# Kernel tuning notes

Measured on AMD Instinct MI355X. Metric: run time of the kernel, lower is better.

## Reference

```python
import jax, jax.numpy as jnp
import numpy as np

B, L, D, DFF, MODES = 16, 1536, 512, 2048, 64
KERNELS = (3, 5, 7)


def setup_inputs() -> dict:
    key = jax.random.key(0)
    ks = jax.random.split(key, 12)
    scale = 1.0 / (D * D)
    f32 = jnp.float32
    return {
        "x": jax.random.normal(ks[0], (B, L, D), f32),
        "w_real": scale * jax.random.normal(ks[1], (D, D, MODES), f32),
        "w_imag": scale * jax.random.normal(ks[2], (D, D, MODES), f32),
        "conv1_w": jax.random.normal(ks[3], (DFF, D), f32) / np.sqrt(D).astype(np.float32),
        "conv2_w": jax.random.normal(ks[4], (D, DFF), f32) / np.sqrt(DFF).astype(np.float32),
        "d1_w1": jax.random.normal(ks[5], (D // 2, D), f32) / np.sqrt(D).astype(np.float32),
        "d1_b1": jnp.zeros((D // 2,), f32),
        "d1_w2": jax.random.normal(ks[6], (len(KERNELS), D // 2), f32) / np.sqrt(D // 2).astype(np.float32),
        "d1_b2": jnp.zeros((len(KERNELS),), f32),
        "d2_w1": jax.random.normal(ks[7], (D // 2, D), f32) / np.sqrt(D).astype(np.float32),
        "d2_b1": jnp.zeros((D // 2,), f32),
        "d2_w2": jax.random.normal(ks[8], (len(KERNELS), D // 2), f32) / np.sqrt(D // 2).astype(np.float32),
        "d2_b2": jnp.zeros((len(KERNELS),), f32),
    }


def _avg_pool1d(x, k):
    # torch AvgPool1d(kernel=k, stride=1, padding=k//2), count_include_pad=True:
    # zero-pad then divide by k everywhere. x: (B, L, D) -> (B, L, D) for odd k.
    pad = k // 2
    xp = jnp.pad(x, ((0, 0), (pad, pad), (0, 0)))
    cs = jnp.pad(jnp.cumsum(xp, axis=1), ((0, 0), (1, 0), (0, 0)))
    return (cs[:, k:, :] - cs[:, :-k, :]) / k


def _moe_decomp(x, w1, b1, w2, b2):
    # trends: (B, L, D, E)
    trends = jnp.stack([_avg_pool1d(x, k) for k in KERNELS], axis=-1)
    h = jax.nn.relu(jnp.einsum("bld,hd->blh", x, w1) + b1)
    logits = jnp.einsum("blh,eh->ble", h, w2) + b2
    gates = jax.nn.softmax(logits, axis=-1)[:, :, None, :]  # (B, L, 1, E)
    x_trend = jnp.sum(trends * gates, axis=-1)
    return x - x_trend  # seasonal component


def _fourier_block(x, w_real, w_imag):
    q_ft = jnp.fft.rfft(x, axis=1)  # (B, L//2+1, D) complex
    modes = min(MODES, q_ft.shape[1])
    weights = (w_real + 1j * w_imag).astype(jnp.complex64)  # (D, D, modes)
    # batched complex matmul over the kept modes (fuses the per-mode loop)
    out_m = jnp.einsum("bmd,dem->bme", q_ft[:, :modes, :], weights[:, :, :modes])
    out_ft = jnp.zeros((x.shape[0], x.shape[1] // 2 + 1, x.shape[2]), jnp.complex64)
    out_ft = out_ft.at[:, :modes, :].set(out_m)
    return jnp.fft.irfft(out_ft, n=x.shape[1], axis=1)


def reference(x, w_real, w_imag, conv1_w, conv2_w,
              d1_w1, d1_b1, d1_w2, d1_b2,
              d2_w1, d2_b1, d2_w2, d2_b2):
    # FEB-f + residual (dropout = identity in eval)
    x = x + _fourier_block(x, w_real, w_imag)
    x = _moe_decomp(x, d1_w1, d1_b1, d1_w2, d1_b2)
    # 1x1 conv FFN == per-token linear layers
    y = jax.nn.relu(jnp.einsum("bld,fd->blf", x, conv1_w))
    y = jnp.einsum("blf,df->bld", y, conv2_w)
    res = _moe_decomp(x + y, d2_w1, d2_b1, d2_w2, d2_b2)
    return res
```

## Files before the change

### kernel.cpp

```cpp
#include <hip/hip_runtime.h>

#define B_   16
#define L_   1536
#define D_   512
#define DFF_ 2048
#define NM   64
#define HID  256

typedef short short8  __attribute__((ext_vector_type(8)));
typedef short short4v __attribute__((ext_vector_type(4)));
typedef float f32x4   __attribute__((ext_vector_type(4)));

__device__ __forceinline__ float b2f(short s) {
  unsigned int u = ((unsigned int)(unsigned short)s) << 16;
  float f; __builtin_memcpy(&f, &u, 4); return f;
}
__device__ __forceinline__ short f2b(float f) {
  unsigned int u; __builtin_memcpy(&u, &f, 4);
  u += 0x7fffu + ((u >> 16) & 1u);
  return (short)(u >> 16);
}
__device__ __forceinline__ f32x4 zero4() {
  f32x4 v; v[0]=0.f; v[1]=0.f; v[2]=0.f; v[3]=0.f; return v;
}

#define MFMA(a,b,c) __builtin_amdgcn_mfma_f32_16x16x32_bf16((a),(b),(c),0,0,0)
#define SWZ(row, grp) (((row) << 6) + ((((grp) ^ ((row) & 7))) << 3))
#define GLDS16(gp, lp) __builtin_amdgcn_global_load_lds( \
    (const __attribute__((address_space(1))) void*)(gp), \
    (__attribute__((address_space(3))) void*)(lp), 16, 0, 0)

__global__ __launch_bounds__(256) void zero_out(float* __restrict__ o, int n) {
  int i = blockIdx.x * 256 + threadIdx.x;
  if (i < n) o[i] = 0.f;
}

__global__ __launch_bounds__(256) void cvt_f32_bf16(const float* __restrict__ s,
                                                    short* __restrict__ d, int n4) {
  int i = blockIdx.x * 256 + threadIdx.x;
  if (i >= n4) return;
  f32x4 v = ((const f32x4*)s)[i];
  short4v o;
  #pragma unroll
  for (int j = 0; j < 4; ++j) o[j] = f2b(v[j]);
  ((short4v*)d)[i] = o;
}

__global__ __launch_bounds__(256) void build_tcs(short* __restrict__ tcs) {
  int i = blockIdx.x * 256 + threadIdx.x;
  if (i >= 128 * L_) return;
  int m = i / L_, l = i - m * L_;
  int mm = (m < 64) ? m : (m - 64);
  int r = (mm * l) % L_;
  float th = (float)r * (6.283185307179586f / (float)L_);
  float s, c; __sincosf(th, &s, &c);
  tcs[i] = f2b((m < 64) ? c : -s);
}
__global__ __launch_bounds__(256) void build_basis(short* __restrict__ basis) {
  int i = blockIdx.x * 256 + threadIdx.x;
  if (i >= L_ * 128) return;
  int l = i >> 7, k = i & 127;
  int m = (k < 64) ? k : (k - 64);
  int r = (m * l) % L_;
  float th = (float)r * (6.283185307179586f / (float)L_);
  float s, c; __sincosf(th, &s, &c);
  float v = (k < 64) ? ((m == 0) ? 1.f : 2.f) * (1.f / (float)L_) * c
                     : (-2.f / (float)L_) * s;
  basis[i] = f2b(v);
}

__global__ __launch_bounds__(256) void transpose_w(const float* __restrict__ w,
                                                   short* __restrict__ wt) {
  __shared__ float tile[64][17];
  int dc = blockIdx.x, e = blockIdx.y, t = threadIdx.x;
  int mBase = blockIdx.z * 16;
  {
    int dl = t >> 2, mg = t & 3;
    f32x4 v = *(const f32x4*)(w + ((long)(dc * 64 + dl) * 512 + e) * 64 + mBase + mg * 4);
    tile[dl][mg*4+0] = v[0]; tile[dl][mg*4+1] = v[1];
    tile[dl][mg*4+2] = v[2]; tile[dl][mg*4+3] = v[3];
  }
  __syncthreads();
  if (t < 128) {
    int mr = t >> 3, dg = t & 7;
    short8 o;
    #pragma unroll
    for (int j = 0; j < 8; ++j) o[j] = f2b(tile[dg * 8 + j][mr]);
    *(short8*)(wt + ((long)(mBase + mr) * 512 + e) * 512 + dc * 64 + dg * 8) = o;
  }
}

__global__ __launch_bounds__(256) void transpose_x(const float* __restrict__ x,
                                                   short* __restrict__ xt) {
  __shared__ float tile[64][65];
  int dc = blockIdx.x, lc = blockIdx.y, b = blockIdx.z, t = threadIdx.x;
  const float* xb = x + (long)b * L_ * D_;
  #pragma unroll
  for (int i = 0; i < 4; ++i) {
    int idx = i * 256 + t; int ll = idx >> 4, dg = idx & 15;
    f32x4 v = *(const f32x4*)(xb + (long)(lc * 64 + ll) * D_ + dc * 64 + dg * 4);
    tile[ll][dg*4+0] = v[0]; tile[ll][dg*4+1] = v[1];
    tile[ll][dg*4+2] = v[2]; tile[ll][dg*4+3] = v[3];
  }
  __syncthreads();
  #pragma unroll
  for (int i = 0; i < 2; ++i) {
    int idx = i * 256 + t; int dl = idx >> 3, lg = idx & 7;
    short8 o;
    #pragma unroll
    for (int j = 0; j < 8; ++j) o[j] = f2b(tile[lg * 8 + j][dl]);
    *(short8*)(xt + ((long)b * D_ + dc * 64 + dl) * L_ + lc * 64 + lg * 8) = o;
  }
}

__global__ __launch_bounds__(256) void transpose_q(const short* __restrict__ in,
                                                   short* __restrict__ out) {
  __shared__ short tile[64][72];
  int ct = blockIdx.x, rt = blockIdx.y, t = threadIdx.x;
  int r0 = rt * 64, c0 = ct * 64;
  #pragma unroll
  for (int i = 0; i < 2; ++i) {
    int idx = i * 256 + t; int r = idx >> 3, g = idx & 7;
    short8 v = *(const short8*)(in + (long)(r0 + r) * 128 + c0 + g * 8);
    #pragma unroll
    for (int j = 0; j < 8; ++j) tile[r][g * 8 + j] = v[j];
  }
  __syncthreads();
  #pragma unroll
  for (int i = 0; i < 2; ++i) {
    int idx = i * 256 + t; int c = idx >> 3, g = idx & 7;
    short8 o;
    #pragma unroll
    for (int j = 0; j < 8; ++j) o[j] = tile[g * 8 + j][c];
    *(short8*)(out + (long)(c0 + c) * 8192 + r0 + g * 8) = o;
  }
}

template<bool RELU, bool HASBIAS>
__global__ __launch_bounds__(256) void gemm64(
    const short* __restrict__ A, long ldA,
    const short* __restrict__ W, long ldW,
    const float* __restrict__ bias,
    short* __restrict__ outB, long ldC, int K)
{
  __shared__ short lA[64 * 64];
  __shared__ short lW[64 * 64];
  const int t = threadIdx.x, lane = t & 63, wid = t >> 6;
  const int quad = lane >> 4, l15 = lane & 15;
  const int wm = (wid & 1) * 32, wn = (wid >> 1) * 32;
  const long row0 = (long)blockIdx.x * 64, col0 = (long)blockIdx.y * 64;
  const short* Ab = A + row0 * ldA;
  const short* Wb = W + col0 * ldW;

  int srcrow[2]; long srcoff[2];
  #pragma unroll
  for (int i = 0; i < 2; ++i) {
    int c = wid * 2 + i;
    int r = c * 8 + (lane >> 3);
    int g = (lane & 7) ^ (r & 7);
    srcrow[i] = r; srcoff[i] = g * 8;
  }

  f32x4 acc[2][2];
  #pragma unroll
  for (int i = 0; i < 2; ++i)
    #pragma unroll
    for (int j = 0; j < 2; ++j) acc[i][j] = zero4();

  for (int k0 = 0; k0 < K; k0 += 64) {
    __syncthreads();
    #pragma unroll
    for (int i = 0; i < 2; ++i) {
      int c = wid * 2 + i;
      GLDS16(Ab + (long)srcrow[i] * ldA + k0 + srcoff[i], lA + c * 512);
      GLDS16(Wb + (long)srcrow[i] * ldW + k0 + srcoff[i], lW + c * 512);
    }
    __syncthreads();
    #pragma unroll
    for (int ks = 0; ks < 2; ++ks) {
      int gq = ks * 4 + quad;
      short8 a0 = *(const short8*)&lA[SWZ(wm + l15, gq)];
      short8 a1 = *(const short8*)&lA[SWZ(wm + 16 + l15, gq)];
      short8 b0 = *(const short8*)&lW[SWZ(wn + l15, gq)];
      short8 b1 = *(const short8*)&lW[SWZ(wn + 16 + l15, gq)];
      acc[0][0] = MFMA(a0, b0, acc[0][0]);
      acc[0][1] = MFMA(a0, b1, acc[0][1]);
      acc[1][0] = MFMA(a1, b0, acc[1][0]);
      acc[1][1] = MFMA(a1, b1, acc[1][1]);
    }
  }
  #pragma unroll
  for (int ni = 0; ni < 2; ++ni) {
    long col = col0 + wn + ni * 16 + l15;
    float bvv = HASBIAS ? bias[col] : 0.f;
    #pragma unroll
    for (int mi = 0; mi < 2; ++mi) {
      #pragma unroll
      for (int r = 0; r < 4; ++r) {
        long row = row0 + wm + mi * 16 + quad * 4 + r;
        float v = acc[mi][ni][r];
        if (HASBIAS) v += bvv;
        if (RELU)    v = fmaxf(v, 0.f);
        outB[row * ldC + col] = f2b(v);
      }
    }
  }
}

template<bool RELU, bool HASBIAS, bool HASRES, bool RESB>
__global__ __launch_bounds__(256) void gemm128(
    const short* __restrict__ A, long ldA, long Az,
    const short* __restrict__ W, long ldW, long Wz,
    const float* __restrict__ bias,
    const void* __restrict__ res, long ldres, long resZ,
    short* __restrict__ outB, long ldC, long Cz, int K)
{
  __shared__ short lA[128 * 64];
  __shared__ short lW[128 * 64];
  const int t = threadIdx.x, lane = t & 63, wid = t >> 6;
  const int quad = lane >> 4, l15 = lane & 15;
  const int wm = (wid & 1) * 64, wn = (wid >> 1) * 64;
  const long row0 = (long)blockIdx.x * 128, col0 = (long)blockIdx.y * 128;
  const int z = blockIdx.z;
  const short* Ab = A + (long)z * Az + row0 * ldA;
  const short* Wb = W + (long)z * Wz + col0 * ldW;

  int srcrow[4]; long srcoff[4];
  #pragma unroll
  for (int i = 0; i < 4; ++i) {
    int c = wid * 4 + i;
    int r = c * 8 + (lane >> 3);
    int g = (lane & 7) ^ (r & 7);
    srcrow[i] = r; srcoff[i] = g * 8;
  }

  f32x4 acc[4][4];
  #pragma unroll
  for (int i = 0; i < 4; ++i)
    #pragma unroll
    for (int j = 0; j < 4; ++j) acc[i][j] = zero4();

  for (int k0 = 0; k0 < K; k0 += 64) {
    __syncthreads();
    #pragma unroll
    for (int i = 0; i < 4; ++i) {
      int c = wid * 4 + i;
      GLDS16(Ab + (long)srcrow[i] * ldA + k0 + srcoff[i], lA + c * 512);
      GLDS16(Wb + (long)srcrow[i] * ldW + k0 + srcoff[i], lW + c * 512);
    }
    __syncthreads();
    #pragma unroll
    for (int ks = 0; ks < 2; ++ks) {
      int gq = ks * 4 + quad;
      short8 av[4], bv[4];
      #pragma unroll
      for (int mi = 0; mi < 4; ++mi) av[mi] = *(const short8*)&lA[SWZ(wm + mi * 16 + l15, gq)];
      #pragma unroll
      for (int ni = 0; ni < 4; ++ni) bv[ni] = *(const short8*)&lW[SWZ(wn + ni * 16 + l15, gq)];
      #pragma unroll
      for (int mi = 0; mi < 4; ++mi)
        #pragma unroll
        for (int ni = 0; ni < 4; ++ni)
          acc[mi][ni] = MFMA(av[mi], bv[ni], acc[mi][ni]);
    }
  }
  #pragma unroll
  for (int ni = 0; ni < 4; ++ni) {
    long col = col0 + wn + ni * 16 + l15;
    float bvv = HASBIAS ? bias[col] : 0.f;
    #pragma unroll
    for (int mi = 0; mi < 4; ++mi) {
      #pragma unroll
      for (int r = 0; r < 4; ++r) {
        long row = row0 + wm + mi * 16 + quad * 4 + r;
        float v = acc[mi][ni][r];
        if (HASBIAS) v += bvv;
        if (RELU)    v = fmaxf(v, 0.f);
        if (HASRES) {
          long ro = (long)z * resZ + row * ldres + col;
          v += RESB ? b2f(((const short*)res)[ro]) : ((const float*)res)[ro];
        }
        outB[(long)z * Cz + row * ldC + col] = f2b(v);
      }
    }
  }
}

__global__ __launch_bounds__(256) void mode_gemm(
    const short* __restrict__ qr, const short* __restrict__ qi,
    const short* __restrict__ wr, const short* __restrict__ wi,
    short* __restrict__ outm)
{
  __shared__ short lqr[16 * 64], lqi[16 * 64], lwr[64 * 64], lwi[64 * 64];
  const int m = blockIdx.x, en = blockIdx.y;
  const int t = threadIdx.x, lane = t & 63, wid = t >> 6;
  const int quad = lane >> 4, l15 = lane & 15;
  const short* qrb = qr + (long)m * (B_ * D_);
  const short* qib = qi + (long)m * (B_ * D_);
  const short* wrb = wr + (long)m * (D_ * D_) + (long)en * 64 * D_;
  const short* wib = wi + (long)m * (D_ * D_) + (long)en * 64 * D_;
  f32x4 accr = zero4(), acci = zero4();
  for (int k0 = 0; k0 < D_; k0 += 64) {
    __syncthreads();
    {
      int idx = t & 127; int r = idx >> 3, cg = idx & 7;
      const short* src = (t < 128 ? qrb : qib) + r * D_ + k0 + cg * 8;
      short* dst = (t < 128) ? lqr : lqi;
      *(short8*)&dst[SWZ(r, cg)] = *(const short8*)src;
    }
    #pragma unroll
    for (int i = 0; i < 4; ++i) {
      int idx = i * 256 + t;
      int which = idx >> 9, idx2 = idx & 511;
      int r = idx2 >> 3, cg = idx2 & 7;
      const short* src = (which ? wib : wrb) + r * D_ + k0 + cg * 8;
      short* dst = which ? lwi : lwr;
      *(short8*)&dst[SWZ(r, cg)] = *(const short8*)src;
    }
    __syncthreads();
    #pragma unroll
    for (int ks = 0; ks < 2; ++ks) {
      int gq = ks * 4 + quad;
      short8 ar = *(const short8*)&lqr[SWZ(l15, gq)];
      short8 ai = *(const short8*)&lqi[SWZ(l15, gq)];
      short8 br = *(const short8*)&lwr[SWZ(wid * 16 + l15, gq)];
      short8 bi = *(const short8*)&lwi[SWZ(wid * 16 + l15, gq)];
      short8 nai;
      #pragma unroll
      for (int j = 0; j < 8; ++j) nai[j] = (short)(ai[j] ^ (short)0x8000);
      accr = MFMA(ar, br, accr);
      accr = MFMA(nai, bi, accr);
      acci = MFMA(ar, bi, acci);
      acci = MFMA(ai, br, acci);
    }
  }
  #pragma unroll
  for (int r = 0; r < 4; ++r) {
    int bb = quad * 4 + r;
    long e = (long)en * 64 + wid * 16 + l15;
    long base = ((long)bb * D_ + e) * 128 + m;
    outm[base]      = f2b(accr[r]);
    outm[base + 64] = f2b(acci[r]);
  }
}

__global__ __launch_bounds__(256) void gates_kernel(
    const short* __restrict__ h, const float* __restrict__ w2,
    const float* __restrict__ b2, float* __restrict__ g, int rows)
{
  int wid = threadIdx.x >> 6, lane = threadIdx.x & 63;
  int row = blockIdx.x * 4 + wid;
  if (row >= rows) return;
  const short* hr = h + (long)row * HID;
  short4v hh = *(const short4v*)(hr + lane * 4);
  float hv[4];
  #pragma unroll
  for (int j = 0; j < 4; ++j) hv[j] = b2f(hh[j]);
  float lg[3];
  #pragma unroll
  for (int e = 0; e < 3; ++e) {
    const float* wrow = w2 + e * HID + lane * 4;
    float p = hv[0] * wrow[0] + hv[1] * wrow[1] + hv[2] * wrow[2] + hv[3] * wrow[3];
    #pragma unroll
    for (int off = 32; off >= 1; off >>= 1) p += __shfl_xor(p, off);
    lg[e] = p + b2[e];
  }
  float mx = fmaxf(lg[0], fmaxf(lg[1], lg[2]));
  float e0 = __expf(lg[0] - mx), e1 = __expf(lg[1] - mx), e2 = __expf(lg[2] - mx);
  float inv = 1.f / (e0 + e1 + e2);
  float gv = (lane == 0) ? e0 * inv : (lane == 1) ? e1 * inv : e2 * inv;
  if (lane < 3) g[(long)row * 3 + lane] = gv;
}

template<bool OUTF, bool WRITEB>
__global__ __launch_bounds__(512) void combine_kernel(
    const short* __restrict__ xin, const float* __restrict__ g,
    float* __restrict__ outf, short* __restrict__ outb)
{
  int lc = blockIdx.x, b = blockIdx.y, d = threadIdx.x;
  int l0 = lc * 64;
  const short* xb = xin + (long)b * L_ * D_ + d;
  const float* gb = g + (long)b * L_ * 3;
  float win[7];
  #pragma unroll
  for (int j = 0; j < 6; ++j) {
    int l = l0 - 3 + j;
    win[j] = (l >= 0 && l < L_) ? b2f(xb[(long)l * D_]) : 0.f;
  }
  for (int i = 0; i < 64; ++i) {
    int lcn = l0 + i;
    int lr = lcn + 3;
    win[6] = (lr < L_) ? b2f(xb[(long)lr * D_]) : 0.f;
    float s3 = win[2] + win[3] + win[4];
    float s5 = s3 + win[1] + win[5];
    float s7 = s5 + win[0] + win[6];
    float g0 = gb[lcn * 3 + 0], g1 = gb[lcn * 3 + 1], g2 = gb[lcn * 3 + 2];
    float trend = g0 * s3 * (1.f / 3.f) + g1 * s5 * (1.f / 5.f) + g2 * s7 * (1.f / 7.f);
    float v = win[3] - trend;
    long o = ((long)b * L_ + lcn) * D_ + d;
    if (OUTF)   outf[o] = v;
    if (WRITEB) outb[o] = f2b(v);
    #pragma unroll
    for (int j = 0; j < 6; ++j) win[j] = win[j + 1];
  }
}

extern "C" void kernel_launch(void* const* d_in, const int* in_sizes, int n_in,
                              void* d_out, int out_size, void* d_ws, size_t ws_size,
                              hipStream_t stream) {
  const float* x       = (const float*)d_in[0];
  const float* w_real  = (const float*)d_in[1];
  const float* w_imag  = (const float*)d_in[2];
  const float* conv1_w = (const float*)d_in[3];
  const float* conv2_w = (const float*)d_in[4];
  const float* d1_w1   = (const float*)d_in[5];
  const float* d1_b1   = (const float*)d_in[6];
  const float* d1_w2   = (const float*)d_in[7];
  const float* d1_b2   = (const float*)d_in[8];
  const float* d2_w1   = (const float*)d_in[9];
  const float* d2_b1   = (const float*)d_in[10];
  const float* d2_w2   = (const float*)d_in[11];
  const float* d2_b2   = (const float*)d_in[12];
  float* OUT = (float*)d_out;

  const size_t REQ_BIG = 144703488, REQ_SMALL = 98566144;
  if (ws_size < REQ_SMALL) {
    zero_out<<<(out_size + 255) / 256, 256, 0, stream>>>(OUT, out_size);
    return;
  }
  const bool big = (ws_size >= REQ_BIG);

  char* ws = (char*)d_ws;
  short* C1WB  = (short*)(ws + 0);
  short* C2WB  = (short*)(ws + 2097152);
  short* D1W1B = (short*)(ws + 4194304);
  short* D2W1B = (short*)(ws + 4456448);
  short* TCS   = (short*)(ws + 4718592);
  short* BASIS = (short*)(ws + 5111808);
  float* G     = (float*)(ws + 5505024);
  short* XT    = (short*)(ws + 6291456);
  short* QRI   = XT;
  short* Y1    = XT;
  short* QT    = (short*)(ws + 31457280);
  short* OUTM  = (short*)(ws + 33554432);
  short* WTR   = (short*)(ws + 35651584);
  short* X1B   = WTR;
  short* WTI   = (short*)(ws + 69206016);
  short* X2B   = (short*)(ws + (big ? 106954752 : 60817408));
  short* H     = (short*)(ws + (big ? 132120576 : 85983232));

  cvt_f32_bf16<<<(262144 + 255) / 256, 256, 0, stream>>>(conv1_w, C1WB, 262144);
  cvt_f32_bf16<<<(262144 + 255) / 256, 256, 0, stream>>>(conv2_w, C2WB, 262144);
  cvt_f32_bf16<<<(32768 + 255) / 256, 256, 0, stream>>>(d1_w1, D1W1B, 32768);
  cvt_f32_bf16<<<(32768 + 255) / 256, 256, 0, stream>>>(d2_w1, D2W1B, 32768);
  build_tcs<<<(128 * L_ + 255) / 256, 256, 0, stream>>>(TCS);
  build_basis<<<(L_ * 128 + 255) / 256, 256, 0, stream>>>(BASIS);
  transpose_w<<<dim3(8, 512, 4), 256, 0, stream>>>(w_real, WTR);
  transpose_w<<<dim3(8, 512, 4), 256, 0, stream>>>(w_imag, WTI);
  transpose_x<<<dim3(8, 24, 16), 256, 0, stream>>>(x, XT);

  gemm64<false, false><<<dim3(128, 2), 256, 0, stream>>>(
      XT, L_, TCS, L_, nullptr, QT, 128, L_);
  transpose_q<<<dim3(2, 128), 256, 0, stream>>>(QT, QRI);

  mode_gemm<<<dim3(64, 8), 256, 0, stream>>>(QRI, QRI + 64 * B_ * D_, WTR, WTI, OUTM);

  gemm128<false, false, true, false><<<dim3(12, 4, 16), 256, 0, stream>>>(
      BASIS, 128, 0, OUTM, 128, (long)D_ * 128, nullptr,
      x, D_, (long)L_ * D_, X1B, D_, (long)L_ * D_, 128);

  gemm64<true, true><<<dim3(384, 4), 256, 0, stream>>>(
      X1B, D_, D1W1B, D_, d1_b1, H, HID, D_);
  gates_kernel<<<6144, 256, 0, stream>>>(H, d1_w2, d1_b2, G, B_ * L_);
  combine_kernel<false, true><<<dim3(24, 16), 512, 0, stream>>>(X1B, G, nullptr, X2B);

  {
    const int nchunk = big ? 1 : 2;
    const long rows = big ? 24576 : 12288;
    for (int rc = 0; rc < nchunk; ++rc) {
      short* Ain = X2B + (long)rc * rows * D_;
      gemm128<true, false, false, false><<<dim3(rows / 128, 16, 1), 256, 0, stream>>>(
          Ain, D_, 0, C1WB, D_, 0, nullptr, nullptr, 0, 0, Y1, DFF_, 0, D_);
      gemm128<false, false, true, true><<<dim3(rows / 128, 4, 1), 256, 0, stream>>>(
          Y1, DFF_, 0, C2WB, DFF_, 0, nullptr, Ain, D_, 0, Ain, D_, 0, DFF_);
    }
  }

  gemm64<true, true><<<dim3(384, 4), 256, 0, stream>>>(
      X2B, D_, D2W1B, D_, d2_b1, H, HID, D_);
  gates_kernel<<<6144, 256, 0, stream>>>(H, d2_w2, d2_b2, G, B_ * L_);
  combine_kernel<true, false><<<dim3(24, 16), 512, 0, stream>>>(X2B, G, OUT, nullptr);
}
```

Baseline: 634.0 us.

## Fuse prep kernels, gate computation into combine, and drop transpose_q via strided stores

Merges the weight conversions and DFT-basis builds into one launch, and merges the real and imaginary weight transposes into a single launch. The gemm64 epilogue gets separate row and column output strides, so the DFT projection writes the transposed layout directly and the transpose_q kernel is no longer needed. The gating softmax is folded into combine_kernel through a shared-memory gate table, which removes gates_kernel and its G buffer. The aim is fewer launches and less intermediate traffic. The cost is uncoalesced strided stores in the DFT gemm and a serial gate prologue in each combine block.

```diff
diff --git a/kernel.cpp b/kernel.cpp
--- a/kernel.cpp
+++ b/kernel.cpp
@@ -35,45 +35,60 @@
   if (i < n) o[i] = 0.f;
 }
 
-__global__ __launch_bounds__(256) void cvt_f32_bf16(const float* __restrict__ s,
-                                                    short* __restrict__ d, int n4) {
-  int i = blockIdx.x * 256 + threadIdx.x;
-  if (i >= n4) return;
-  f32x4 v = ((const f32x4*)s)[i];
-  short4v o;
-  #pragma unroll
-  for (int j = 0; j < 4; ++j) o[j] = f2b(v[j]);
-  ((short4v*)d)[i] = o;
-}
-
-__global__ __launch_bounds__(256) void build_tcs(short* __restrict__ tcs) {
-  int i = blockIdx.x * 256 + threadIdx.x;
-  if (i >= 128 * L_) return;
-  int m = i / L_, l = i - m * L_;
-  int mm = (m < 64) ? m : (m - 64);
-  int r = (mm * l) % L_;
-  float th = (float)r * (6.283185307179586f / (float)L_);
-  float s, c; __sincosf(th, &s, &c);
-  tcs[i] = f2b((m < 64) ? c : -s);
-}
-__global__ __launch_bounds__(256) void build_basis(short* __restrict__ basis) {
-  int i = blockIdx.x * 256 + threadIdx.x;
-  if (i >= L_ * 128) return;
-  int l = i >> 7, k = i & 127;
-  int m = (k < 64) ? k : (k - 64);
-  int r = (m * l) % L_;
-  float th = (float)r * (6.283185307179586f / (float)L_);
-  float s, c; __sincosf(th, &s, &c);
-  float v = (k < 64) ? ((m == 0) ? 1.f : 2.f) * (1.f / (float)L_) * c
-                     : (-2.f / (float)L_) * s;
-  basis[i] = f2b(v);
-}
-
-__global__ __launch_bounds__(256) void transpose_w(const float* __restrict__ w,
-                                                   short* __restrict__ wt) {
+__global__ __launch_bounds__(256) void prep_all(
+    const float* __restrict__ conv1_w, const float* __restrict__ conv2_w,
+    const float* __restrict__ d1_w1,  const float* __restrict__ d2_w1,
+    short* __restrict__ c1, short* __restrict__ c2,
+    short* __restrict__ dw1, short* __restrict__ dw2,
+    short* __restrict__ tcs, short* __restrict__ basis)
+{
+  int blk = blockIdx.x;
+  if (blk < 2304) {
+    const float* s; short* d; int i;
+    if (blk < 1024)      { s = conv1_w; d = c1;  i = blk * 256 + threadIdx.x; }
+    else if (blk < 2048) { s = conv2_w; d = c2;  i = (blk - 1024) * 256 + threadIdx.x; }
+    else if (blk < 2176) { s = d1_w1;   d = dw1; i = (blk - 2048) * 256 + threadIdx.x; }
+    else                 { s = d2_w1;   d = dw2; i = (blk - 2176) * 256 + threadIdx.x; }
+    f32x4 v = ((const f32x4*)s)[i];
+    short4v o;
+    #pragma unroll
+    for (int j = 0; j < 4; ++j) o[j] = f2b(v[j]);
+    ((short4v*)d)[i] = o;
+    return;
+  }
+  if (blk < 3072) {
+    int i = (blk - 2304) * 256 + threadIdx.x;
+    int m = i / L_, l = i - m * L_;
+    int mm = (m < 64) ? m : (m - 64);
+    int r = (mm * l) % L_;
+    float th = (float)r * (6.283185307179586f / (float)L_);
+    float s, c; __sincosf(th, &s, &c);
+    tcs[i] = f2b((m < 64) ? c : -s);
+    return;
+  }
+  {
+    int i = (blk - 3072) * 256 + threadIdx.x;
+    int l = i >> 7, k = i & 127;
+    int m = (k < 64) ? k : (k - 64);
+    int r = (m * l) % L_;
+    float th = (float)r * (6.283185307179586f / (float)L_);
+    float s, c; __sincosf(th, &s, &c);
+    float v = (k < 64) ? ((m == 0) ? 1.f : 2.f) * (1.f / (float)L_) * c
+                       : (-2.f / (float)L_) * s;
+    basis[i] = f2b(v);
+  }
+}
+
+__global__ __launch_bounds__(256) void transpose_w(
+    const float* __restrict__ wre, const float* __restrict__ wim,
+    short* __restrict__ wtr, short* __restrict__ wti)
+{
   __shared__ float tile[64][17];
   int dc = blockIdx.x, e = blockIdx.y, t = threadIdx.x;
-  int mBase = blockIdx.z * 16;
+  int zz = blockIdx.z;
+  const float* w = (zz < 4) ? wre : wim;
+  short* wt      = (zz < 4) ? wtr : wti;
+  int mBase = (zz & 3) * 16;
   {
     int dl = t >> 2, mg = t & 3;
     f32x4 v = *(const f32x4*)(w + ((long)(dc * 64 + dl) * 512 + e) * 64 + mBase + mg * 4);
@@ -113,35 +128,12 @@
   }
 }
 
-__global__ __launch_bounds__(256) void transpose_q(const short* __restrict__ in,
-                                                   short* __restrict__ out) {
-  __shared__ short tile[64][72];
-  int ct = blockIdx.x, rt = blockIdx.y, t = threadIdx.x;
-  int r0 = rt * 64, c0 = ct * 64;
-  #pragma unroll
-  for (int i = 0; i < 2; ++i) {
-    int idx = i * 256 + t; int r = idx >> 3, g = idx & 7;
-    short8 v = *(const short8*)(in + (long)(r0 + r) * 128 + c0 + g * 8);
-    #pragma unroll
-    for (int j = 0; j < 8; ++j) tile[r][g * 8 + j] = v[j];
-  }
-  __syncthreads();
-  #pragma unroll
-  for (int i = 0; i < 2; ++i) {
-    int idx = i * 256 + t; int c = idx >> 3, g = idx & 7;
-    short8 o;
-    #pragma unroll
-    for (int j = 0; j < 8; ++j) o[j] = tile[g * 8 + j][c];
-    *(short8*)(out + (long)(c0 + c) * 8192 + r0 + g * 8) = o;
-  }
-}
-
 template<bool RELU, bool HASBIAS>
 __global__ __launch_bounds__(256) void gemm64(
     const short* __restrict__ A, long ldA,
     const short* __restrict__ W, long ldW,
     const float* __restrict__ bias,
-    short* __restrict__ outB, long ldC, int K)
+    short* __restrict__ outB, long csr, long csc, int K)
 {
   __shared__ short lA[64 * 64];
   __shared__ short lW[64 * 64];
@@ -201,7 +193,7 @@
         float v = acc[mi][ni][r];
         if (HASBIAS) v += bvv;
         if (RELU)    v = fmaxf(v, 0.f);
-        outB[row * ldC + col] = f2b(v);
+        outB[row * csr + col * csc] = f2b(v);
       }
     }
   }
@@ -344,43 +336,43 @@
   }
 }
 
-__global__ __launch_bounds__(256) void gates_kernel(
-    const short* __restrict__ h, const float* __restrict__ w2,
-    const float* __restrict__ b2, float* __restrict__ g, int rows)
-{
-  int wid = threadIdx.x >> 6, lane = threadIdx.x & 63;
-  int row = blockIdx.x * 4 + wid;
-  if (row >= rows) return;
-  const short* hr = h + (long)row * HID;
-  short4v hh = *(const short4v*)(hr + lane * 4);
-  float hv[4];
-  #pragma unroll
-  for (int j = 0; j < 4; ++j) hv[j] = b2f(hh[j]);
-  float lg[3];
-  #pragma unroll
-  for (int e = 0; e < 3; ++e) {
-    const float* wrow = w2 + e * HID + lane * 4;
-    float p = hv[0] * wrow[0] + hv[1] * wrow[1] + hv[2] * wrow[2] + hv[3] * wrow[3];
-    #pragma unroll
-    for (int off = 32; off >= 1; off >>= 1) p += __shfl_xor(p, off);
-    lg[e] = p + b2[e];
-  }
-  float mx = fmaxf(lg[0], fmaxf(lg[1], lg[2]));
-  float e0 = __expf(lg[0] - mx), e1 = __expf(lg[1] - mx), e2 = __expf(lg[2] - mx);
-  float inv = 1.f / (e0 + e1 + e2);
-  float gv = (lane == 0) ? e0 * inv : (lane == 1) ? e1 * inv : e2 * inv;
-  if (lane < 3) g[(long)row * 3 + lane] = gv;
-}
-
 template<bool OUTF, bool WRITEB>
 __global__ __launch_bounds__(512) void combine_kernel(
-    const short* __restrict__ xin, const float* __restrict__ g,
+    const short* __restrict__ xin, const short* __restrict__ h,
+    const float* __restrict__ w2, const float* __restrict__ b2,
     float* __restrict__ outf, short* __restrict__ outb)
 {
-  int lc = blockIdx.x, b = blockIdx.y, d = threadIdx.x;
+  __shared__ float lG[64][4];
+  int lc = blockIdx.x, b = blockIdx.y, t = threadIdx.x;
+  int wid = t >> 6, lane = t & 63;
   int l0 = lc * 64;
+  #pragma unroll
+  for (int pi = 0; pi < 8; ++pi) {
+    int pos = wid * 8 + pi;
+    long row = (long)b * L_ + l0 + pos;
+    short4v hh = *(const short4v*)(h + row * HID + lane * 4);
+    float hv[4];
+    #pragma unroll
+    for (int j = 0; j < 4; ++j) hv[j] = b2f(hh[j]);
+    float lg[3];
+    #pragma unroll
+    for (int e = 0; e < 3; ++e) {
+      const float* wrow = w2 + e * HID + lane * 4;
+      float p = hv[0] * wrow[0] + hv[1] * wrow[1] + hv[2] * wrow[2] + hv[3] * wrow[3];
+      #pragma unroll
+      for (int off = 32; off >= 1; off >>= 1) p += __shfl_xor(p, off);
+      lg[e] = p + b2[e];
+    }
+    float mx = fmaxf(lg[0], fmaxf(lg[1], lg[2]));
+    float e0 = __expf(lg[0] - mx), e1 = __expf(lg[1] - mx), e2 = __expf(lg[2] - mx);
+    float inv = 1.f / (e0 + e1 + e2);
+    float gv = (lane == 0) ? e0 * inv : (lane == 1) ? e1 * inv : e2 * inv;
+    if (lane < 3) lG[pos][lane] = gv;
+  }
+  __syncthreads();
+
+  int d = t;
   const short* xb = xin + (long)b * L_ * D_ + d;
-  const float* gb = g + (long)b * L_ * 3;
   float win[7];
   #pragma unroll
   for (int j = 0; j < 6; ++j) {
@@ -394,8 +386,8 @@
     float s3 = win[2] + win[3] + win[4];
     float s5 = s3 + win[1] + win[5];
     float s7 = s5 + win[0] + win[6];
-    float g0 = gb[lcn * 3 + 0], g1 = gb[lcn * 3 + 1], g2 = gb[lcn * 3 + 2];
-    float trend = g0 * s3 * (1.f / 3.f) + g1 * s5 * (1.f / 5.f) + g2 * s7 * (1.f / 7.f);
+    float trend = lG[i][0] * s3 * (1.f / 3.f) + lG[i][1] * s5 * (1.f / 5.f)
+                + lG[i][2] * s7 * (1.f / 7.f);
     float v = win[3] - trend;
     long o = ((long)b * L_ + lcn) * D_ + d;
     if (OUTF)   outf[o] = v;
@@ -437,11 +429,9 @@
   short* D2W1B = (short*)(ws + 4456448);
   short* TCS   = (short*)(ws + 4718592);
   short* BASIS = (short*)(ws + 5111808);
-  float* G     = (float*)(ws + 5505024);
   short* XT    = (short*)(ws + 6291456);
-  short* QRI   = XT;
   short* Y1    = XT;
-  short* QT    = (short*)(ws + 31457280);
+  short* QRI   = (short*)(ws + 31457280);
   short* OUTM  = (short*)(ws + 33554432);
   short* WTR   = (short*)(ws + 35651584);
   short* X1B   = WTR;
@@ -449,19 +439,13 @@
   short* X2B   = (short*)(ws + (big ? 106954752 : 60817408));
   short* H     = (short*)(ws + (big ? 132120576 : 85983232));
 
-  cvt_f32_bf16<<<(262144 + 255) / 256, 256, 0, stream>>>(conv1_w, C1WB, 262144);
-  cvt_f32_bf16<<<(262144 + 255) / 256, 256, 0, stream>>>(conv2_w, C2WB, 262144);
-  cvt_f32_bf16<<<(32768 + 255) / 256, 256, 0, stream>>>(d1_w1, D1W1B, 32768);
-  cvt_f32_bf16<<<(32768 + 255) / 256, 256, 0, stream>>>(d2_w1, D2W1B, 32768);
-  build_tcs<<<(128 * L_ + 255) / 256, 256, 0, stream>>>(TCS);
-  build_basis<<<(L_ * 128 + 255) / 256, 256, 0, stream>>>(BASIS);
-  transpose_w<<<dim3(8, 512, 4), 256, 0, stream>>>(w_real, WTR);
-  transpose_w<<<dim3(8, 512, 4), 256, 0, stream>>>(w_imag, WTI);
+  prep_all<<<3840, 256, 0, stream>>>(conv1_w, conv2_w, d1_w1, d2_w1,
+                                     C1WB, C2WB, D1W1B, D2W1B, TCS, BASIS);
+  transpose_w<<<dim3(8, 512, 8), 256, 0, stream>>>(w_real, w_imag, WTR, WTI);
   transpose_x<<<dim3(8, 24, 16), 256, 0, stream>>>(x, XT);
 
   gemm64<false, false><<<dim3(128, 2), 256, 0, stream>>>(
-      XT, L_, TCS, L_, nullptr, QT, 128, L_);
-  transpose_q<<<dim3(2, 128), 256, 0, stream>>>(QT, QRI);
+      XT, L_, TCS, L_, nullptr, QRI, 1, (long)B_ * D_, L_);
 
   mode_gemm<<<dim3(64, 8), 256, 0, stream>>>(QRI, QRI + 64 * B_ * D_, WTR, WTI, OUTM);
 
@@ -470,9 +454,9 @@
       x, D_, (long)L_ * D_, X1B, D_, (long)L_ * D_, 128);
 
   gemm64<true, true><<<dim3(384, 4), 256, 0, stream>>>(
-      X1B, D_, D1W1B, D_, d1_b1, H, HID, D_);
-  gates_kernel<<<6144, 256, 0, stream>>>(H, d1_w2, d1_b2, G, B_ * L_);
-  combine_kernel<false, true><<<dim3(24, 16), 512, 0, stream>>>(X1B, G, nullptr, X2B);
+      X1B, D_, D1W1B, D_, d1_b1, H, HID, 1, D_);
+  combine_kernel<false, true><<<dim3(24, 16), 512, 0, stream>>>(
+      X1B, H, d1_w2, d1_b2, nullptr, X2B);
 
   {
     const int nchunk = big ? 1 : 2;
@@ -487,7 +471,7 @@
   }
 
   gemm64<true, true><<<dim3(384, 4), 256, 0, stream>>>(
-      X2B, D_, D2W1B, D_, d2_b1, H, HID, D_);
-  gates_kernel<<<6144, 256, 0, stream>>>(H, d2_w2, d2_b2, G, B_ * L_);
-  combine_kernel<true, false><<<dim3(24, 16), 512, 0, stream>>>(X2B, G, OUT, nullptr);
-}
+      X2B, D_, D2W1B, D_, d2_b1, H, HID, 1, D_);
+  combine_kernel<true, false><<<dim3(24, 16), 512, 0, stream>>>(
+      X2B, H, d2_w2, d2_b2, OUT, nullptr);
+}
```

Measured after the change: 624.6 us. Within noise of the previous version (-1.5%).
